# Optimization experiments

Hardware: AMD Instinct MI355X
Metric: run time of the kernel (lower is better)

## Reference

```python
import jax, jax.numpy as jnp
import numpy as np

B, N, K, D = 256, 64, 12, 128


def setup_inputs() -> dict:
    key = jax.random.key(0)
    ks = jax.random.split(key, 12)
    s = 1.0 / np.sqrt(D)
    inp = {
        "nodes_hidden": jax.random.normal(ks[0], (B, N, D), jnp.float32),
        "neighbors_hidden": jax.random.normal(ks[1], (B, N, K, D), jnp.float32),
        # binary neighbor-validity mask (float, as in the torch code)
        "mask": (jax.random.uniform(ks[2], (B, N, K)) < 0.7).astype(jnp.float32),
        "Wq": jax.random.uniform(ks[3], (D, D), jnp.float32, -s, s),
        "bq": jax.random.uniform(ks[4], (D,), jnp.float32, -s, s),
        "Wk": jax.random.uniform(ks[5], (D, D), jnp.float32, -s, s),
        "bk": jax.random.uniform(ks[6], (D,), jnp.float32, -s, s),
        "Wv": jax.random.uniform(ks[7], (D, D), jnp.float32, -s, s),
        "bv": jax.random.uniform(ks[8], (D,), jnp.float32, -s, s),
        # W_att: Linear(2D -> 1); split into the query half and key half of its weight
        "wa_q": jax.random.uniform(ks[9], (D,), jnp.float32, -s, s),
        "wa_k": jax.random.uniform(ks[10], (D,), jnp.float32, -s, s),
        "ba": jax.random.uniform(ks[11], (), jnp.float32, -s, s),
    }
    return inp


def reference(nodes_hidden, neighbors_hidden, mask, Wq, bq, Wk, bk, Wv, bv, wa_q, wa_k, ba):
    # prepend the node itself to its neighbor list: [B,N,K+1,D]
    nh = jnp.concatenate([nodes_hidden[:, :, None, :], neighbors_hidden], axis=2)
    # prepend an always-valid slot to the mask: [B,N,K+1]
    m = jnp.concatenate([jnp.ones(mask.shape[:-1] + (1,), mask.dtype), mask], axis=-1)

    q = nodes_hidden @ Wq + bq            # [B,N,D]
    k = nh @ Wk + bk                      # [B,N,K+1,D]
    v = nh @ Wv + bv                      # [B,N,K+1,D]

    # W_att(cat([q,k])) == q.wa_q + k.wa_k + ba  (avoids materializing the 2D concat)
    sim = (q @ wa_q)[:, :, None] + k @ wa_k + ba   # [B,N,K+1]
    sim = jnp.where(sim >= 0, sim, 0.2 * sim)      # LeakyReLU(0.2)
    sim = jnp.exp(sim) * m                         # masked exp (matches torch exactly)
    attn = sim / (jnp.sum(sim, axis=-1, keepdims=True) + 1e-16)
    return jnp.einsum('bnk,bnkd->bnd', attn, v)    # [B,N,D]
```

## Files before the change

kernel.cpp:

```cpp
#include <hip/hip_runtime.h>


#define B_  256
#define N_  64
#define K_  12
#define D_  128
#define BN  (B_ * N_)

#define WS_HBAR   512
#define WS_SCALE  (512 + BN * D_)

__global__ void prep_kernel(const float* __restrict__ Wq, const float* __restrict__ bq,
                            const float* __restrict__ Wk, const float* __restrict__ bk,
                            const float* __restrict__ wa_q, const float* __restrict__ wa_k,
                            float* __restrict__ ws) {
    int g = blockIdx.x;
    int l = threadIdx.x;
    const float* row;
    const float* wa;
    float* outp;
    if (g < 128)      { row = Wq + g * D_;         wa = wa_q; outp = ws + g; }
    else if (g < 256) { row = Wk + (g - 128) * D_; wa = wa_k; outp = ws + 128 + (g - 128); }
    else if (g == 256){ row = bq;                  wa = wa_q; outp = ws + 256; }
    else              { row = bk;                  wa = wa_k; outp = ws + 257; }

    float2 r = ((const float2*)row)[l];
    float2 w = ((const float2*)wa)[l];
    float p = r.x * w.x + r.y * w.y;
    #pragma unroll
    for (int m = 1; m < 64; m <<= 1) p += __shfl_xor(p, m, 64);
    if (l == 0) *outp = p;
}

__global__ void __launch_bounds__(256)
attn_kernel(const float* __restrict__ nodes, const float* __restrict__ neigh,
            const float* __restrict__ mask, const float* __restrict__ ba_p,
            float* __restrict__ ws) {
    const int wave = threadIdx.x >> 6;
    const int l    = threadIdx.x & 63;
    const int idx  = blockIdx.x * 4 + wave;

    const float cq  = ws[256];
    const float ckb = ws[257];
    const float ba  = ba_p[0];
    float2 wqe = ((const float2*)ws)[l];
    float2 wke = ((const float2*)(ws + 128))[l];

    const float2* np = (const float2*)(nodes + (size_t)idx * D_);
    const float2* gp = (const float2*)(neigh + (size_t)idx * K_ * D_);

    float2 x[K_ + 1];
    x[0] = np[l];
    #pragma unroll
    for (int j = 0; j < K_; ++j) x[j + 1] = gp[j * 64 + l];

    float mval = (l < K_) ? mask[(size_t)idx * K_ + l] : 0.0f;

    float pq = x[0].x * wqe.x + x[0].y * wqe.y;
    float pk[K_ + 1];
    #pragma unroll
    for (int j = 0; j <= K_; ++j) pk[j] = x[j].x * wke.x + x[j].y * wke.y;

    #pragma unroll
    for (int m = 1; m < 64; m <<= 1) {
        pq += __shfl_xor(pq, m, 64);
        #pragma unroll
        for (int j = 0; j <= K_; ++j) pk[j] += __shfl_xor(pk[j], m, 64);
    }

    const float aq = pq + cq;
    float e[K_ + 1];
    float S = 0.0f;
    #pragma unroll
    for (int j = 0; j <= K_; ++j) {
        float s = aq + pk[j] + ckb + ba;
        s = (s >= 0.0f) ? s : 0.2f * s;
        float mj = (j == 0) ? 1.0f : __shfl(mval, j - 1, 64);
        e[j] = expf(s) * mj;
        S += e[j];
    }
    const float inv = 1.0f / (S + 1e-16f);

    float h0 = 0.0f, h1 = 0.0f;
    #pragma unroll
    for (int j = 0; j <= K_; ++j) {
        float w = e[j] * inv;
        h0 += w * x[j].x;
        h1 += w * x[j].y;
    }

    float2* hb = (float2*)(ws + WS_HBAR) + (size_t)idx * (D_ / 2);
    hb[l] = make_float2(h0, h1);
    if (l == 0) ws[WS_SCALE + idx] = S * inv;
}

#define HB_STRIDE 132
__global__ void __launch_bounds__(256)
gemm_kernel(const float* __restrict__ ws, const float* __restrict__ Wv,
            const float* __restrict__ bv, float* __restrict__ out) {
    __shared__ float hb[32 * HB_STRIDE];
    __shared__ float scL[32];

    const int t    = threadIdx.x;
    const int row0 = blockIdx.x * 32;
    const float* hbar  = ws + WS_HBAR;
    const float* scale = ws + WS_SCALE;

    #pragma unroll
    for (int i = 0; i < 4; ++i) {
        int idx = (i * 256 + t) * 4;
        int row = idx >> 7;
        int k   = idx & 127;
        float4 v = *(const float4*)(hbar + (size_t)(row0 + row) * D_ + k);
        *(float4*)(hb + row * HB_STRIDE + k) = v;
    }
    if (t < 32) scL[t] = scale[row0 + t];
    __syncthreads();

    const int rg = t >> 5;
    const int cg = t & 31;
    const float4* wv4 = (const float4*)Wv;

    float acc[4][4];
    #pragma unroll
    for (int i = 0; i < 4; ++i)
        #pragma unroll
        for (int c = 0; c < 4; ++c) acc[i][c] = 0.0f;

    #pragma unroll 8
    for (int k = 0; k < D_; ++k) {
        float4 b = wv4[k * 32 + cg];
        #pragma unroll
        for (int i = 0; i < 4; ++i) {
            float a = hb[(rg * 4 + i) * HB_STRIDE + k];
            acc[i][0] += a * b.x;
            acc[i][1] += a * b.y;
            acc[i][2] += a * b.z;
            acc[i][3] += a * b.w;
        }
    }

    float4 bvv = ((const float4*)bv)[cg];
    #pragma unroll
    for (int i = 0; i < 4; ++i) {
        float s = scL[rg * 4 + i];
        float4 o;
        o.x = acc[i][0] + bvv.x * s;
        o.y = acc[i][1] + bvv.y * s;
        o.z = acc[i][2] + bvv.z * s;
        o.w = acc[i][3] + bvv.w * s;
        *(float4*)(out + (size_t)(row0 + rg * 4 + i) * D_ + cg * 4) = o;
    }
}

extern "C" void kernel_launch(void* const* d_in, const int* in_sizes, int n_in,
                              void* d_out, int out_size, void* d_ws, size_t ws_size,
                              hipStream_t stream) {
    const float* nodes = (const float*)d_in[0];
    const float* neigh = (const float*)d_in[1];
    const float* mask  = (const float*)d_in[2];
    const float* Wq    = (const float*)d_in[3];
    const float* bq    = (const float*)d_in[4];
    const float* Wk    = (const float*)d_in[5];
    const float* bk    = (const float*)d_in[6];
    const float* Wv    = (const float*)d_in[7];
    const float* bv    = (const float*)d_in[8];
    const float* wa_q  = (const float*)d_in[9];
    const float* wa_k  = (const float*)d_in[10];
    const float* ba    = (const float*)d_in[11];
    float* out = (float*)d_out;
    float* ws  = (float*)d_ws;

    prep_kernel<<<258, 64, 0, stream>>>(Wq, bq, Wk, bk, wa_q, wa_k, ws);
    attn_kernel<<<BN / 4, 256, 0, stream>>>(nodes, neigh, mask, ba, ws);
    gemm_kernel<<<BN / 32, 256, 0, stream>>>(ws, Wv, bv, out);
}
```

Measured before the change: 197.0 us.

## Fuse attention aggregation and Wv GEMM into one kernel via shared memory

Merges the attention kernel and the Wv projection GEMM into one kernel. Each block computes 32 rows of attention-weighted hidden states directly into shared memory, with every wave handling 8 rows in sequence, and then runs the 32x128 GEMM. This drops the global-memory round trip for the intermediate and one kernel launch, and also switches expf to __expf. In exchange there are 8x fewer blocks during the bandwidth-heavy attention phase, and each wave processes its rows serially, which may reduce memory-level parallelism.

```diff
diff --git a/kernel.cpp b/kernel.cpp
--- a/kernel.cpp
+++ b/kernel.cpp
@@ -6,9 +6,6 @@
 #define K_  12
 #define D_  128
 #define BN  (B_ * N_)
-
-#define WS_HBAR   512
-#define WS_SCALE  (512 + BN * D_)
 
 __global__ void prep_kernel(const float* __restrict__ Wq, const float* __restrict__ bq,
                             const float* __restrict__ Wk, const float* __restrict__ bk,
@@ -32,93 +29,81 @@
     if (l == 0) *outp = p;
 }
 
+#define HB_STRIDE 132
 __global__ void __launch_bounds__(256)
-attn_kernel(const float* __restrict__ nodes, const float* __restrict__ neigh,
-            const float* __restrict__ mask, const float* __restrict__ ba_p,
-            float* __restrict__ ws) {
-    const int wave = threadIdx.x >> 6;
-    const int l    = threadIdx.x & 63;
-    const int idx  = blockIdx.x * 4 + wave;
+fused_kernel(const float* __restrict__ nodes, const float* __restrict__ neigh,
+             const float* __restrict__ mask, const float* __restrict__ ba_p,
+             const float* __restrict__ ws, const float* __restrict__ Wv,
+             const float* __restrict__ bv, float* __restrict__ out) {
+    __shared__ float hb[32 * HB_STRIDE];
+    __shared__ float scL[32];
+
+    const int t    = threadIdx.x;
+    const int wave = t >> 6;
+    const int l    = t & 63;
 
     const float cq  = ws[256];
     const float ckb = ws[257];
     const float ba  = ba_p[0];
+    const float cst = cq + ckb + ba;
     float2 wqe = ((const float2*)ws)[l];
     float2 wke = ((const float2*)(ws + 128))[l];
 
-    const float2* np = (const float2*)(nodes + (size_t)idx * D_);
-    const float2* gp = (const float2*)(neigh + (size_t)idx * K_ * D_);
+    for (int p = 0; p < 8; ++p) {
+        const int lrow = wave * 8 + p;
+        const int idx  = blockIdx.x * 32 + lrow;
 
-    float2 x[K_ + 1];
-    x[0] = np[l];
-    #pragma unroll
-    for (int j = 0; j < K_; ++j) x[j + 1] = gp[j * 64 + l];
+        const float2* np = (const float2*)(nodes + (size_t)idx * D_);
+        const float2* gp = (const float2*)(neigh + (size_t)idx * K_ * D_);
 
-    float mval = (l < K_) ? mask[(size_t)idx * K_ + l] : 0.0f;
+        float2 x[K_ + 1];
+        x[0] = np[l];
+        #pragma unroll
+        for (int j = 0; j < K_; ++j) x[j + 1] = gp[j * 64 + l];
 
-    float pq = x[0].x * wqe.x + x[0].y * wqe.y;
-    float pk[K_ + 1];
-    #pragma unroll
-    for (int j = 0; j <= K_; ++j) pk[j] = x[j].x * wke.x + x[j].y * wke.y;
+        float mval = (l < K_) ? mask[(size_t)idx * K_ + l] : 0.0f;
 
-    #pragma unroll
-    for (int m = 1; m < 64; m <<= 1) {
-        pq += __shfl_xor(pq, m, 64);
+        float pq = x[0].x * wqe.x + x[0].y * wqe.y;
+        float pk[K_ + 1];
         #pragma unroll
-        for (int j = 0; j <= K_; ++j) pk[j] += __shfl_xor(pk[j], m, 64);
+        for (int j = 0; j <= K_; ++j) pk[j] = x[j].x * wke.x + x[j].y * wke.y;
+
+        #pragma unroll
+        for (int m = 1; m < 64; m <<= 1) {
+            pq += __shfl_xor(pq, m, 64);
+            #pragma unroll
+            for (int j = 0; j <= K_; ++j) pk[j] += __shfl_xor(pk[j], m, 64);
+        }
+
+        const float base = pq + cst;
+        float e[K_ + 1];
+        float S = 0.0f;
+        #pragma unroll
+        for (int j = 0; j <= K_; ++j) {
+            float s = base + pk[j];
+            s = (s >= 0.0f) ? s : 0.2f * s;
+            float mj = (j == 0) ? 1.0f : __shfl(mval, j - 1, 64);
+            e[j] = __expf(s) * mj;
+            S += e[j];
+        }
+        const float inv = 1.0f / (S + 1e-16f);
+
+        float h0 = 0.0f, h1 = 0.0f;
+        #pragma unroll
+        for (int j = 0; j <= K_; ++j) {
+            float w = e[j] * inv;
+            h0 += w * x[j].x;
+            h1 += w * x[j].y;
+        }
+
+        *(float2*)(hb + lrow * HB_STRIDE + 2 * l) = make_float2(h0, h1);
+        if (l == 0) scL[lrow] = S * inv;
     }
-
-    const float aq = pq + cq;
-    float e[K_ + 1];
-    float S = 0.0f;
-    #pragma unroll
-    for (int j = 0; j <= K_; ++j) {
-        float s = aq + pk[j] + ckb + ba;
-        s = (s >= 0.0f) ? s : 0.2f * s;
-        float mj = (j == 0) ? 1.0f : __shfl(mval, j - 1, 64);
-        e[j] = expf(s) * mj;
-        S += e[j];
-    }
-    const float inv = 1.0f / (S + 1e-16f);
-
-    float h0 = 0.0f, h1 = 0.0f;
-    #pragma unroll
-    for (int j = 0; j <= K_; ++j) {
-        float w = e[j] * inv;
-        h0 += w * x[j].x;
-        h1 += w * x[j].y;
-    }
-
-    float2* hb = (float2*)(ws + WS_HBAR) + (size_t)idx * (D_ / 2);
-    hb[l] = make_float2(h0, h1);
-    if (l == 0) ws[WS_SCALE + idx] = S * inv;
-}
-
-#define HB_STRIDE 132
-__global__ void __launch_bounds__(256)
-gemm_kernel(const float* __restrict__ ws, const float* __restrict__ Wv,
-            const float* __restrict__ bv, float* __restrict__ out) {
-    __shared__ float hb[32 * HB_STRIDE];
-    __shared__ float scL[32];
-
-    const int t    = threadIdx.x;
-    const int row0 = blockIdx.x * 32;
-    const float* hbar  = ws + WS_HBAR;
-    const float* scale = ws + WS_SCALE;
-
-    #pragma unroll
-    for (int i = 0; i < 4; ++i) {
-        int idx = (i * 256 + t) * 4;
-        int row = idx >> 7;
-        int k   = idx & 127;
-        float4 v = *(const float4*)(hbar + (size_t)(row0 + row) * D_ + k);
-        *(float4*)(hb + row * HB_STRIDE + k) = v;
-    }
-    if (t < 32) scL[t] = scale[row0 + t];
     __syncthreads();
 
     const int rg = t >> 5;
     const int cg = t & 31;
+    const int row0 = blockIdx.x * 32;
     const float4* wv4 = (const float4*)Wv;
 
     float acc[4][4];
@@ -172,6 +157,5 @@
     float* ws  = (float*)d_ws;
 
     prep_kernel<<<258, 64, 0, stream>>>(Wq, bq, Wk, bk, wa_q, wa_k, ws);
-    attn_kernel<<<BN / 4, 256, 0, stream>>>(nodes, neigh, mask, ba, ws);
-    gemm_kernel<<<BN / 32, 256, 0, stream>>>(ws, Wv, bv, out);
+    fused_kernel<<<BN / 32, 256, 0, stream>>>(nodes, neigh, mask, ba, ws, Wv, bv, out);
 }
```

Measured after the change: 187.5 us. 1.05x faster.
